# Performance work log

Hardware: AMD Instinct MI355X
Metric: run time of the kernel (lower is better)

Reference implementation:

```python
import jax, jax.numpy as jnp
import numpy as np

B, T, S, H, N = 4, 1024, 1024, 1024, 16
D = H // N
EPS = 1e-12
MASK_FILL = -1e6


def setup_inputs() -> dict:
    key = jax.random.key(0)
    ks = jax.random.split(key, 20)
    w = lambda i: jax.random.normal(ks[i], (H, H), jnp.float32) * 0.02
    zb = jnp.zeros((H,), jnp.float32)
    tgt_mask = jnp.tile(jnp.tril(jnp.ones((T, T), jnp.int32))[None], (B, 1, 1))
    return {
        "encoder_states": jax.random.normal(ks[0], (B, S, H), jnp.float32),
        "decoder_inputs": jax.random.normal(ks[1], (B, T, H), jnp.float32),
        "src_attn_mask": jnp.ones((B, S), jnp.int32),
        "tgt_attn_mask": tgt_mask,
        "q_w": w(2), "q_b": zb,
        "k_w": w(3), "k_b": zb,
        "v_w": w(4), "v_b": zb,
        "sq_w": w(5), "sq_b": zb,
        "sk_w": w(6), "sk_b": zb,
        "sv_w": w(7), "sv_b": zb,
        "dense_w": w(8), "dense_b": zb,
        "ln_g": jnp.ones((H,), jnp.float32),
        "ln_b": zb,
    }


def _layernorm(x, g, b):
    mu = jnp.mean(x, -1, keepdims=True)
    var = jnp.mean(jnp.square(x - mu), -1, keepdims=True)
    return (x - mu) * jax.lax.rsqrt(var + EPS) * g + b


def _attention(q, k, v, mask, dense_w, dense_b, ln_g, ln_b):
    # q:[B,Q,H] k,v:[B,K,H]; NOTE: original applies NO 1/sqrt(d) scaling.
    b, qlen, _ = q.shape
    klen = k.shape[1]
    qh = q.reshape(b, qlen, N, D).transpose(0, 2, 1, 3)  # [B,N,Q,D]
    kh = k.reshape(b, klen, N, D).transpose(0, 2, 1, 3)
    vh = v.reshape(b, klen, N, D).transpose(0, 2, 1, 3)
    scores = jnp.einsum('bnqd,bnkd->bnqk', qh, kh)
    m = mask.reshape(b, 1, qlen, klen) if mask.ndim == 3 else mask.reshape(b, 1, 1, klen)
    scores = jnp.where(m == 0, jnp.asarray(MASK_FILL, scores.dtype), scores)
    probs = jax.nn.softmax(scores, axis=-1)  # dropout = identity at eval
    ctx = jnp.einsum('bnqk,bnkd->bqnd', probs, vh)  # [B,Q,N,D]
    w = dense_w.T.reshape(N, D, H)
    proj = jnp.einsum('bqnd,ndh->bqh', ctx, w) + dense_b
    # Residual is q (the query projection), faithful to the original code.
    return _layernorm(q + proj, ln_g, ln_b)


def reference(encoder_states, decoder_inputs, src_attn_mask, tgt_attn_mask,
              q_w, q_b, k_w, k_b, v_w, v_b,
              sq_w, sq_b, sk_w, sk_b, sv_w, sv_b,
              dense_w, dense_b, ln_g, ln_b):
    lin = lambda x, w, b: x @ w.T + b
    # self-attention over decoder inputs
    q = lin(decoder_inputs, q_w, q_b)
    k = lin(decoder_inputs, k_w, k_b)
    v = lin(decoder_inputs, v_w, v_b)
    self_out = _attention(q, k, v, tgt_attn_mask, dense_w, dense_b, ln_g, ln_b)
    # cross-attention into encoder states (same dense/LayerNorm modules)
    q2 = lin(self_out, sq_w, sq_b)
    k2 = lin(encoder_states, sk_w, sk_b)
    v2 = lin(encoder_states, sv_w, sv_b)
    return _attention(q2, k2, v2, src_attn_mask, dense_w, dense_b, ln_g, ln_b)
```

## Files before the change

kernel.cpp:

```cpp
#include <hip/hip_runtime.h>

typedef __attribute__((ext_vector_type(4))) float f32x4;
typedef __attribute__((ext_vector_type(8))) short bf16x8;

#define GVOID const __attribute__((address_space(1))) void
#define LVOID __attribute__((address_space(3))) void

__device__ __forceinline__ float bf2f(ushort u){
  union { float f; unsigned int i; } c; c.i = ((unsigned int)u) << 16; return c.f;
}
__device__ __forceinline__ ushort f2bf(float f){
  union { float f; unsigned int i; } c; c.f = f;
  unsigned int r = (c.i + 0x7FFFu + ((c.i >> 16) & 1u)) >> 16;
  return (ushort)r;
}

struct CvtArgs {
  const float* s[9];
  ushort*      d[9];
  int          blks[9];
};
__global__ __launch_bounds__(256) void cvtk_multi(CvtArgs ca){
  int bid = blockIdx.x;
  int seg = 0, base = 0;
  while (bid - base >= ca.blks[seg]){ base += ca.blks[seg]; ++seg; }
  int i = ((bid - base) * 256 + threadIdx.x) * 4;
  float4 v = *(const float4*)(ca.s[seg] + i);
  ushort4 o;
  o.x = f2bf(v.x); o.y = f2bf(v.y); o.z = f2bf(v.z); o.w = f2bf(v.w);
  *(ushort4*)(ca.d[seg] + i) = o;
}

struct GemmArgs {
  const ushort* A[3];
  const ushort* W[3];
  const float*  bias[3];
  const ushort* R[3];
  ushort*       C[3];
  int           mode[3];
};

__global__ __launch_bounds__(256,2) void gemm128(GemmArgs ga, int nmat, int N, int K){
  __shared__ ushort As[128 * 64];
  __shared__ ushort Bs[128 * 64];
  const int ntn = N >> 7;
  const int per = ntn * nmat;
  const int x = blockIdx.x & 7, ii = blockIdx.x >> 3;
  const int ipx = gridDim.x >> 3;
  const int gpx = ipx / per;
  const int tm = x * gpx + ii / per;
  const int q = ii % per;
  const int g = q / ntn, tn = q % ntn;
  const ushort* __restrict__ A = ga.A[g];
  const ushort* __restrict__ W = ga.W[g];
  const float*  __restrict__ bias = ga.bias[g];
  const ushort* __restrict__ R = ga.R[g];
  ushort* __restrict__ C = ga.C[g];
  const int mode = ga.mode[g];

  const int t = threadIdx.x, lane = t & 63, wave = t >> 6;
  const int wr = wave >> 1, wc = wave & 1;
  const int l15 = lane & 15, l4 = lane >> 4;
  const int rowBase = tm * 128, colBase = tn * 128;

  f32x4 acc[4][4] = {};
  const int NT = K >> 6;
  for (int tk = 0; tk < NT; ++tk){
    const int k0 = tk * 64;
    __syncthreads();
#pragma unroll
    for (int j = 0; j < 4; ++j){
      int cb = j * 256 + wave * 64 + lane;
      int row = cb >> 3;
      int kc = (cb & 7) ^ (row & 7);
      const ushort* srcA = A + (size_t)(rowBase + row) * K + k0 + kc * 8;
      __builtin_amdgcn_global_load_lds((GVOID*)srcA, (LVOID*)(As + (size_t)cb * 8), 16, 0, 0);
      const ushort* srcB = W + (size_t)(colBase + row) * K + k0 + kc * 8;
      __builtin_amdgcn_global_load_lds((GVOID*)srcB, (LVOID*)(Bs + (size_t)cb * 8), 16, 0, 0);
    }
    __syncthreads();
#pragma unroll
    for (int kk = 0; kk < 2; ++kk){
      bf16x8 a[4], b[4];
#pragma unroll
      for (int m = 0; m < 4; ++m){
        int row = wr * 64 + m * 16 + l15;
        int ch = row * 8 + ((kk * 4 + l4) ^ (row & 7));
        a[m] = *(const bf16x8*)(As + ch * 8);
      }
#pragma unroll
      for (int n = 0; n < 4; ++n){
        int row = wc * 64 + n * 16 + l15;
        int ch = row * 8 + ((kk * 4 + l4) ^ (row & 7));
        b[n] = *(const bf16x8*)(Bs + ch * 8);
      }
#pragma unroll
      for (int m = 0; m < 4; ++m)
#pragma unroll
      for (int n = 0; n < 4; ++n)
        acc[m][n] = __builtin_amdgcn_mfma_f32_16x16x32_bf16(a[m], b[n], acc[m][n], 0, 0, 0);
    }
  }
#pragma unroll
  for (int m = 0; m < 4; ++m)
#pragma unroll
  for (int n = 0; n < 4; ++n)
#pragma unroll
  for (int r = 0; r < 4; ++r){
    int row = rowBase + wr * 64 + m * 16 + l4 * 4 + r;
    int col = colBase + wc * 64 + n * 16 + l15;
    float v = acc[m][n][r] + bias[col];
    if (mode == 1) v += bf2f(R[(size_t)row * N + col]);
    if (mode == 2){
      int bb = row >> 10, tt = row & 1023, nh = col >> 6, d = col & 63;
      C[((size_t)((bb * 16 + nh) * 64 + d)) * 1024 + tt] = f2bf(v);
    } else {
      C[(size_t)row * N + col] = f2bf(v);
    }
  }
}

__global__ __launch_bounds__(256,2) void gemm_bt(GemmArgs ga, int nmat, int M, int N, int K){
  __shared__ ushort As[2][128 * 64];
  __shared__ ushort Bs[2][64 * 64];
  const int nb = gridDim.x;
  const int ntn = N >> 6;
  const int tq_cnt = ntn * nmat;
  const int x = blockIdx.x & 7, ii = blockIdx.x >> 3;
  const int ipx = nb >> 3;
  const int gpx = ipx / tq_cnt;
  const int tm = x * gpx + ii / tq_cnt;
  const int tq = ii % tq_cnt;
  const int g = tq / ntn, tn = tq % ntn;
  const ushort* __restrict__ A = ga.A[g];
  const ushort* __restrict__ W = ga.W[g];
  const float*  __restrict__ bias = ga.bias[g];
  const ushort* __restrict__ R = ga.R[g];
  ushort* __restrict__ C = ga.C[g];
  const int mode = ga.mode[g];

  const int t = threadIdx.x, lane = t & 63, wave = t >> 6;
  const int wr = wave >> 1, wc = wave & 1;
  const int l15 = lane & 15, l4 = lane >> 4;
  const int rowBase = tm * 128, colBase = tn * 64;

  auto stage = [&](int buf, int k0){
#pragma unroll
    for (int j = 0; j < 4; ++j){
      int cb = j * 256 + wave * 64;
      int p = cb + lane;
      int row = p >> 3;
      int kc = (p & 7) ^ (row & 7);
      const ushort* src = A + (size_t)(rowBase + row) * K + k0 + kc * 8;
      __builtin_amdgcn_global_load_lds((GVOID*)src, (LVOID*)(&As[buf][cb * 8]), 16, 0, 0);
    }
#pragma unroll
    for (int j = 0; j < 2; ++j){
      int cb = j * 256 + wave * 64;
      int p = cb + lane;
      int row = p >> 3;
      int kc = (p & 7) ^ (row & 7);
      const ushort* src = W + (size_t)(colBase + row) * K + k0 + kc * 8;
      __builtin_amdgcn_global_load_lds((GVOID*)src, (LVOID*)(&Bs[buf][cb * 8]), 16, 0, 0);
    }
  };

  f32x4 acc[4][2] = {};
  const int NT = K >> 6;
  stage(0, 0);
  __syncthreads();
  for (int tk = 0; tk < NT; ++tk){
    const int cur = tk & 1;
    if (tk + 1 < NT) stage(cur ^ 1, (tk + 1) * 64);
#pragma unroll
    for (int kk = 0; kk < 2; ++kk){
      bf16x8 a[4], b[2];
#pragma unroll
      for (int m = 0; m < 4; ++m){
        int row = wr * 64 + m * 16 + l15;
        int ch = row * 8 + kk * 4 + l4;
        ch ^= (row & 7);
        a[m] = *(const bf16x8*)(&As[cur][ch * 8]);
      }
#pragma unroll
      for (int n = 0; n < 2; ++n){
        int row = wc * 32 + n * 16 + l15;
        int ch = row * 8 + kk * 4 + l4;
        ch ^= (row & 7);
        b[n] = *(const bf16x8*)(&Bs[cur][ch * 8]);
      }
#pragma unroll
      for (int m = 0; m < 4; ++m)
#pragma unroll
      for (int n = 0; n < 2; ++n)
        acc[m][n] = __builtin_amdgcn_mfma_f32_16x16x32_bf16(a[m], b[n], acc[m][n], 0, 0, 0);
    }
    __syncthreads();
  }
#pragma unroll
  for (int m = 0; m < 4; ++m)
#pragma unroll
  for (int n = 0; n < 2; ++n)
#pragma unroll
  for (int r = 0; r < 4; ++r){
    int row = rowBase + wr * 64 + m * 16 + l4 * 4 + r;
    int col = colBase + wc * 32 + n * 16 + l15;
    float v = acc[m][n][r] + bias[col];
    if (mode == 1) v += bf2f(R[(size_t)row * N + col]);
    if (mode == 2){
      int bb = row >> 10, tt = row & 1023, nh = col >> 6, d = col & 63;
      C[((size_t)((bb * 16 + nh) * 64 + d)) * 1024 + tt] = f2bf(v);
    } else {
      C[(size_t)row * N + col] = f2bf(v);
    }
  }
}

__global__ __launch_bounds__(256,2) void attn_kernel(const ushort* __restrict__ Q, const ushort* __restrict__ Kv,
    const ushort* __restrict__ Vt, ushort* __restrict__ O, const int* __restrict__ smask, int causal){
  __shared__ ushort Ks[2][64 * 64];
  __shared__ ushort Vs[2][64 * 64];
  __shared__ __align__(16) char Ps[4][4096];
  const int p = blockIdx.x;
  const int x = p & 7, j = p >> 3;
  const int gg = x * 8 + (j & 7);
  const int b = gg >> 4, head = gg & 15;
  const int c3 = (j >> 3) & 3, rr = j >> 5;
  const int qt = causal ? (rr ? (7 - c3) : c3) : (j >> 3);
  const int t = threadIdx.x, lane = t & 63, wave = t >> 6;
  const int l15 = lane & 15, l4 = lane >> 4;
  const int qr0 = qt * 128 + wave * 32;
  const int sw = (l15 & 7) << 3;

  bf16x8 aq[2][2];
#pragma unroll
  for (int m = 0; m < 2; ++m)
#pragma unroll
  for (int kk = 0; kk < 2; ++kk)
    aq[m][kk] = *(const bf16x8*)(Q + (size_t)(b * 1024 + qr0 + m * 16 + l15) * 1024 + head * 64 + kk * 32 + l4 * 8);

  f32x4 cacc[2][4] = {};
  float mrow[2] = {-1e30f, -1e30f}, lrow[2] = {0.f, 0.f};

  auto stage = [&](int buf, int k0){
#pragma unroll
    for (int jj = 0; jj < 2; ++jj){
      int cb = jj * 256 + wave * 64;
      int pp = cb + lane;
      int row = pp >> 3;
      int kc = (pp & 7) ^ (row & 7);
      const ushort* src = Kv + (size_t)(b * 1024 + k0 + row) * 1024 + head * 64 + kc * 8;
      __builtin_amdgcn_global_load_lds((GVOID*)src, (LVOID*)(&Ks[buf][cb * 8]), 16, 0, 0);
    }
#pragma unroll
    for (int jj = 0; jj < 2; ++jj){
      int cb = jj * 256 + wave * 64;
      int pp = cb + lane;
      int row = pp >> 3;
      int kc = (pp & 7) ^ (row & 7);
      const ushort* src = Vt + (size_t)((b * 16 + head) * 64 + row) * 1024 + k0 + kc * 8;
      __builtin_amdgcn_global_load_lds((GVOID*)src, (LVOID*)(&Vs[buf][cb * 8]), 16, 0, 0);
    }
  };

  const int nkt = causal ? (2 * qt + 2) : 16;
  stage(0, 0);
  __syncthreads();
  char* Pb = &Ps[wave][0];
  for (int kt = 0; kt < nkt; ++kt){
    const int cur = kt & 1;
    const int k0 = kt * 64;
    if (kt + 1 < nkt) stage(cur ^ 1, (kt + 1) * 64);
    const ushort* Kb_ = &Ks[cur][0];
    const ushort* Vb_ = &Vs[cur][0];
    f32x4 st[2][4] = {};
#pragma unroll
    for (int kk = 0; kk < 2; ++kk){
      bf16x8 ak[4];
#pragma unroll
      for (int n = 0; n < 4; ++n){
        int row = n * 16 + l15;
        int ch = row * 8 + ((kk * 4 + l4) ^ (row & 7));
        ak[n] = *(const bf16x8*)(Kb_ + ch * 8);
      }
#pragma unroll
      for (int m = 0; m < 2; ++m)
#pragma unroll
      for (int n = 0; n < 4; ++n)
        st[m][n] = __builtin_amdgcn_mfma_f32_16x16x32_bf16(ak[n], aq[m][kk], st[m][n], 0, 0, 0);
    }
    if (causal && k0 + 63 > qr0){
#pragma unroll
      for (int m = 0; m < 2; ++m)
#pragma unroll
      for (int n = 0; n < 4; ++n)
#pragma unroll
      for (int r = 0; r < 4; ++r)
        if (k0 + n * 16 + l4 * 4 + r > qr0 + m * 16 + l15) st[m][n][r] = -1e6f;
    }
    if (smask){
#pragma unroll
      for (int n = 0; n < 4; ++n)
#pragma unroll
      for (int r = 0; r < 4; ++r){
        int mv = smask[b * 1024 + k0 + n * 16 + l4 * 4 + r];
        if (mv == 0){ st[0][n][r] = -1e6f; st[1][n][r] = -1e6f; }
      }
    }
    float scal[2];
#pragma unroll
    for (int m = 0; m < 2; ++m){
      float mx = st[m][0][0];
#pragma unroll
      for (int n = 0; n < 4; ++n)
#pragma unroll
      for (int r = 0; r < 4; ++r) mx = fmaxf(mx, st[m][n][r]);
      mx = fmaxf(mx, __shfl_xor(mx, 16));
      mx = fmaxf(mx, __shfl_xor(mx, 32));
      float mn = fmaxf(mrow[m], mx);
      scal[m] = __expf(mrow[m] - mn);
      mrow[m] = mn;
      float ps = 0.f;
#pragma unroll
      for (int n = 0; n < 4; ++n)
#pragma unroll
      for (int r = 0; r < 4; ++r){
        float pv = __expf(st[m][n][r] - mn);
        st[m][n][r] = pv;
        ps += pv;
      }
      ps += __shfl_xor(ps, 16);
      ps += __shfl_xor(ps, 32);
      lrow[m] = lrow[m] * scal[m] + ps;
    }
#pragma unroll
    for (int m = 0; m < 2; ++m)
#pragma unroll
    for (int r = 0; r < 4; ++r){
      float sb = __shfl(scal[m], l4 * 4 + r);
#pragma unroll
      for (int nd = 0; nd < 4; ++nd) cacc[m][nd][r] *= sb;
    }
#pragma unroll
    for (int m = 0; m < 2; ++m)
#pragma unroll
    for (int n = 0; n < 4; ++n){
      unsigned lo = (unsigned)f2bf(st[m][n][0]) | ((unsigned)f2bf(st[m][n][1]) << 16);
      unsigned hi = (unsigned)f2bf(st[m][n][2]) | ((unsigned)f2bf(st[m][n][3]) << 16);
      unsigned long long pk = (unsigned long long)lo | ((unsigned long long)hi << 32);
      *(unsigned long long*)(Pb + m * 2048 + l15 * 128 + ((n * 32 + l4 * 8) ^ sw)) = pk;
    }
#pragma unroll
    for (int ks = 0; ks < 2; ++ks){
      bf16x8 bv[4];
#pragma unroll
      for (int nd = 0; nd < 4; ++nd){
        int row = nd * 16 + l15;
        int ch = row * 8 + ((ks * 4 + l4) ^ (row & 7));
        bv[nd] = *(const bf16x8*)(Vb_ + ch * 8);
      }
#pragma unroll
      for (int m = 0; m < 2; ++m){
        int base = m * 2048 + l15 * 128;
        int o = ks * 64 + l4 * 16;
        union { bf16x8 v; unsigned long long u[2]; } pa;
        pa.u[0] = *(const unsigned long long*)(Pb + base + ((o    ) ^ sw));
        pa.u[1] = *(const unsigned long long*)(Pb + base + ((o + 8) ^ sw));
#pragma unroll
        for (int nd = 0; nd < 4; ++nd)
          cacc[m][nd] = __builtin_amdgcn_mfma_f32_16x16x32_bf16(pa.v, bv[nd], cacc[m][nd], 0, 0, 0);
      }
    }
    __syncthreads();
  }
#pragma unroll
  for (int m = 0; m < 2; ++m)
#pragma unroll
  for (int r = 0; r < 4; ++r){
    float lb = __shfl(lrow[m], l4 * 4 + r);
    float inv = 1.f / lb;
    int row = qr0 + m * 16 + l4 * 4 + r;
#pragma unroll
    for (int nd = 0; nd < 4; ++nd){
      int col = head * 64 + nd * 16 + l15;
      O[(size_t)(b * 1024 + row) * 1024 + col] = f2bf(cacc[m][nd][r] * inv);
    }
  }
}

__global__ __launch_bounds__(256) void ln_kernel(const ushort* __restrict__ X, const float* __restrict__ g,
    const float* __restrict__ bta, ushort* __restrict__ outb, float* __restrict__ outf){
  const int row = blockIdx.x, t = threadIdx.x;
  const ushort* xr = X + (size_t)row * 1024;
  ushort4 u = *(const ushort4*)(xr + t * 4);
  float x0 = bf2f(u.x), x1 = bf2f(u.y), x2 = bf2f(u.z), x3 = bf2f(u.w);
  float s = x0 + x1 + x2 + x3;
  float s2 = x0 * x0 + x1 * x1 + x2 * x2 + x3 * x3;
#pragma unroll
  for (int d = 1; d < 64; d <<= 1){ s += __shfl_xor(s, d); s2 += __shfl_xor(s2, d); }
  __shared__ float red[8];
  const int lane = t & 63, wave = t >> 6;
  if (lane == 0){ red[wave] = s; red[4 + wave] = s2; }
  __syncthreads();
  s = red[0] + red[1] + red[2] + red[3];
  s2 = red[4] + red[5] + red[6] + red[7];
  float mu = s * (1.f / 1024.f);
  float var = fmaxf(s2 * (1.f / 1024.f) - mu * mu, 0.f);
  float rstd = rsqrtf(var + 1e-12f);
  int col = t * 4;
  float y0 = (x0 - mu) * rstd * g[col + 0] + bta[col + 0];
  float y1 = (x1 - mu) * rstd * g[col + 1] + bta[col + 1];
  float y2 = (x2 - mu) * rstd * g[col + 2] + bta[col + 2];
  float y3 = (x3 - mu) * rstd * g[col + 3] + bta[col + 3];
  if (outb){
    ushort4 o; o.x = f2bf(y0); o.y = f2bf(y1); o.z = f2bf(y2); o.w = f2bf(y3);
    *(ushort4*)(outb + (size_t)row * 1024 + col) = o;
  } else {
    float4 o; o.x = y0; o.y = y1; o.z = y2; o.w = y3;
    *(float4*)(outf + (size_t)row * 1024 + col) = o;
  }
}

extern "C" void kernel_launch(void* const* d_in, const int* in_sizes, int n_in,
                              void* d_out, int out_size, void* d_ws, size_t ws_size,
                              hipStream_t stream){
  const float* enc = (const float*)d_in[0];
  const float* dec = (const float*)d_in[1];
  const int* smask = (const int*)d_in[2];
  const float* q_w  = (const float*)d_in[4];  const float* q_b  = (const float*)d_in[5];
  const float* k_w  = (const float*)d_in[6];  const float* k_b  = (const float*)d_in[7];
  const float* v_w  = (const float*)d_in[8];  const float* v_b  = (const float*)d_in[9];
  const float* sq_w = (const float*)d_in[10]; const float* sq_b = (const float*)d_in[11];
  const float* sk_w = (const float*)d_in[12]; const float* sk_b = (const float*)d_in[13];
  const float* sv_w = (const float*)d_in[14]; const float* sv_b = (const float*)d_in[15];
  const float* dw   = (const float*)d_in[16]; const float* db   = (const float*)d_in[17];
  const float* lng  = (const float*)d_in[18]; const float* lnb  = (const float*)d_in[19];
  ushort* ws = (ushort*)d_ws;
  const size_t MEG = 1024u * 1024u;
  ushort* decb = ws + 0 * MEG;
  ushort* encb = ws + 4 * MEG;
  ushort* Qb   = ws + 8 * MEG;
  ushort* Kb   = ws + 12 * MEG;
  ushort* Vtb  = ws + 20 * MEG;
  ushort* ctx  = ws + 24 * MEG;
  ushort* S1   = ws + 28 * MEG;
  ushort* Wq  = ws + 32 * MEG; ushort* Wk  = ws + 33 * MEG; ushort* Wv  = ws + 34 * MEG;
  ushort* Wsq = ws + 35 * MEG; ushort* Wsk = ws + 36 * MEG; ushort* Wsv = ws + 37 * MEG;
  ushort* Wd  = ws + 38 * MEG;
  const int M = 4096, N = 1024, Kd = 1024;
  {
    CvtArgs ca;
    ca.s[0] = dec;  ca.d[0] = decb; ca.blks[0] = 4096;
    ca.s[1] = enc;  ca.d[1] = encb; ca.blks[1] = 4096;
    ca.s[2] = q_w;  ca.d[2] = Wq;   ca.blks[2] = 1024;
    ca.s[3] = k_w;  ca.d[3] = Wk;   ca.blks[3] = 1024;
    ca.s[4] = v_w;  ca.d[4] = Wv;   ca.blks[4] = 1024;
    ca.s[5] = sq_w; ca.d[5] = Wsq;  ca.blks[5] = 1024;
    ca.s[6] = sk_w; ca.d[6] = Wsk;  ca.blks[6] = 1024;
    ca.s[7] = sv_w; ca.d[7] = Wsv;  ca.blks[7] = 1024;
    ca.s[8] = dw;   ca.d[8] = Wd;   ca.blks[8] = 1024;
    cvtk_multi<<<15360, 256, 0, stream>>>(ca);
  }
  {
    GemmArgs ga;
    ga.A[0] = decb; ga.A[1] = decb; ga.A[2] = decb;
    ga.W[0] = Wq;   ga.W[1] = Wk;   ga.W[2] = Wv;
    ga.bias[0] = q_b; ga.bias[1] = k_b; ga.bias[2] = v_b;
    ga.R[0] = nullptr; ga.R[1] = nullptr; ga.R[2] = nullptr;
    ga.C[0] = Qb;   ga.C[1] = Kb;   ga.C[2] = Vtb;
    ga.mode[0] = 0; ga.mode[1] = 0; ga.mode[2] = 2;
    gemm128<<<768, 256, 0, stream>>>(ga, 3, N, Kd);
  }
  attn_kernel<<<512, 256, 0, stream>>>(Qb, Kb, Vtb, ctx, nullptr, 1);
  {
    GemmArgs ga = {};
    ga.A[0] = ctx; ga.W[0] = Wd; ga.bias[0] = db; ga.R[0] = Qb; ga.C[0] = S1; ga.mode[0] = 1;
    gemm_bt<<<512, 256, 0, stream>>>(ga, 1, M, N, Kd);
  }
  ln_kernel<<<4096, 256, 0, stream>>>(S1, lng, lnb, decb, nullptr);
  {
    GemmArgs ga;
    ga.A[0] = decb; ga.A[1] = encb; ga.A[2] = encb;
    ga.W[0] = Wsq;  ga.W[1] = Wsk;  ga.W[2] = Wsv;
    ga.bias[0] = sq_b; ga.bias[1] = sk_b; ga.bias[2] = sv_b;
    ga.R[0] = nullptr; ga.R[1] = nullptr; ga.R[2] = nullptr;
    ga.C[0] = Qb;   ga.C[1] = Kb;   ga.C[2] = Vtb;
    ga.mode[0] = 0; ga.mode[1] = 0; ga.mode[2] = 2;
    gemm128<<<768, 256, 0, stream>>>(ga, 3, N, Kd);
  }
  attn_kernel<<<512, 256, 0, stream>>>(Qb, Kb, Vtb, ctx, smask, 0);
  {
    GemmArgs ga = {};
    ga.A[0] = ctx; ga.W[0] = Wd; ga.bias[0] = db; ga.R[0] = Qb; ga.C[0] = S1; ga.mode[0] = 1;
    gemm_bt<<<512, 256, 0, stream>>>(ga, 1, M, N, Kd);
  }
  ln_kernel<<<4096, 256, 0, stream>>>(S1, lng, lnb, nullptr, (float*)d_out);
}
```

Before: 225.0 us.

## Halve attention query tile, fold log2e into Q projection, use exp2 softmax

Attention blocks now cover 64 query rows instead of 128, with one 16-row slice per wave. The grid doubles to 1024 blocks and launch bounds allow 4 blocks per CU, with a new causal tile ordering for load balance. The Q projection is pre-scaled by log2(e) so softmax can use the hardware exp2 directly; the residual in the dense GEMM is rescaled by ln2 to undo this, and the mask fill becomes -1.5e6 to match. Probabilities are packed with v_cvt_pk_bf16_f32, and the unused residual/transposed-store paths are dropped from the GEMM epilogues. The risk is that each K/V tile is loaded for fewer query rows, and the bf16-rounded scaled Q differs slightly numerically.

```diff
diff --git a/kernel.cpp b/kernel.cpp
--- a/kernel.cpp
+++ b/kernel.cpp
@@ -5,6 +5,9 @@
 
 #define GVOID const __attribute__((address_space(1))) void
 #define LVOID __attribute__((address_space(3))) void
+
+#define LOG2E 1.44269504f
+#define LN2   0.69314718f
 
 __device__ __forceinline__ float bf2f(ushort u){
   union { float f; unsigned int i; } c; c.i = ((unsigned int)u) << 16; return c.f;
@@ -38,6 +41,7 @@
   const ushort* R[3];
   ushort*       C[3];
   int           mode[3];
+  float         scale[3];
 };
 
 __global__ __launch_bounds__(256,2) void gemm128(GemmArgs ga, int nmat, int N, int K){
@@ -54,9 +58,9 @@
   const ushort* __restrict__ A = ga.A[g];
   const ushort* __restrict__ W = ga.W[g];
   const float*  __restrict__ bias = ga.bias[g];
-  const ushort* __restrict__ R = ga.R[g];
   ushort* __restrict__ C = ga.C[g];
   const int mode = ga.mode[g];
+  const float scale = ga.scale[g];
 
   const int t = threadIdx.x, lane = t & 63, wave = t >> 6;
   const int wr = wave >> 1, wc = wave & 1;
@@ -109,8 +113,7 @@
   for (int r = 0; r < 4; ++r){
     int row = rowBase + wr * 64 + m * 16 + l4 * 4 + r;
     int col = colBase + wc * 64 + n * 16 + l15;
-    float v = acc[m][n][r] + bias[col];
-    if (mode == 1) v += bf2f(R[(size_t)row * N + col]);
+    float v = (acc[m][n][r] + bias[col]) * scale;
     if (mode == 2){
       int bb = row >> 10, tt = row & 1023, nh = col >> 6, d = col & 63;
       C[((size_t)((bb * 16 + nh) * 64 + d)) * 1024 + tt] = f2bf(v);
@@ -206,41 +209,38 @@
     int row = rowBase + wr * 64 + m * 16 + l4 * 4 + r;
     int col = colBase + wc * 32 + n * 16 + l15;
     float v = acc[m][n][r] + bias[col];
-    if (mode == 1) v += bf2f(R[(size_t)row * N + col]);
-    if (mode == 2){
-      int bb = row >> 10, tt = row & 1023, nh = col >> 6, d = col & 63;
-      C[((size_t)((bb * 16 + nh) * 64 + d)) * 1024 + tt] = f2bf(v);
-    } else {
-      C[(size_t)row * N + col] = f2bf(v);
-    }
-  }
-}
-
-__global__ __launch_bounds__(256,2) void attn_kernel(const ushort* __restrict__ Q, const ushort* __restrict__ Kv,
+    if (mode == 1) v += bf2f(R[(size_t)row * N + col]) * LN2;
+    C[(size_t)row * N + col] = f2bf(v);
+  }
+}
+
+__global__ __launch_bounds__(256,4) void attn_kernel(const ushort* __restrict__ Q, const ushort* __restrict__ Kv,
     const ushort* __restrict__ Vt, ushort* __restrict__ O, const int* __restrict__ smask, int causal){
   __shared__ ushort Ks[2][64 * 64];
   __shared__ ushort Vs[2][64 * 64];
-  __shared__ __align__(16) char Ps[4][4096];
+  __shared__ __align__(16) char Ps[4][2048];
   const int p = blockIdx.x;
   const int x = p & 7, j = p >> 3;
   const int gg = x * 8 + (j & 7);
   const int b = gg >> 4, head = gg & 15;
-  const int c3 = (j >> 3) & 3, rr = j >> 5;
-  const int qt = causal ? (rr ? (7 - c3) : c3) : (j >> 3);
+  const int rr = j >> 3;
+  int qt;
+  if (causal){
+    int lo = rr & 3, hi = rr >> 2;
+    qt = (hi == 0) ? lo * 2 : (hi == 1) ? lo * 2 + 1 : (hi == 2) ? 15 - lo * 2 : 14 - lo * 2;
+  } else qt = rr;
   const int t = threadIdx.x, lane = t & 63, wave = t >> 6;
   const int l15 = lane & 15, l4 = lane >> 4;
-  const int qr0 = qt * 128 + wave * 32;
+  const int qr0 = qt * 64 + wave * 16;
   const int sw = (l15 & 7) << 3;
 
-  bf16x8 aq[2][2];
-#pragma unroll
-  for (int m = 0; m < 2; ++m)
+  bf16x8 aq[2];
 #pragma unroll
   for (int kk = 0; kk < 2; ++kk)
-    aq[m][kk] = *(const bf16x8*)(Q + (size_t)(b * 1024 + qr0 + m * 16 + l15) * 1024 + head * 64 + kk * 32 + l4 * 8);
-
-  f32x4 cacc[2][4] = {};
-  float mrow[2] = {-1e30f, -1e30f}, lrow[2] = {0.f, 0.f};
+    aq[kk] = *(const bf16x8*)(Q + (size_t)(b * 1024 + qr0 + l15) * 1024 + head * 64 + kk * 32 + l4 * 8);
+
+  f32x4 cacc[4] = {};
+  float mrow = -1e30f, lrow = 0.f;
 
   auto stage = [&](int buf, int k0){
 #pragma unroll
@@ -263,7 +263,7 @@
     }
   };
 
-  const int nkt = causal ? (2 * qt + 2) : 16;
+  const int nkt = causal ? (qt + 1) : 16;
   stage(0, 0);
   __syncthreads();
   char* Pb = &Ps[wave][0];
@@ -273,7 +273,7 @@
     if (kt + 1 < nkt) stage(cur ^ 1, (kt + 1) * 64);
     const ushort* Kb_ = &Ks[cur][0];
     const ushort* Vb_ = &Vs[cur][0];
-    f32x4 st[2][4] = {};
+    f32x4 st[4] = {};
 #pragma unroll
     for (int kk = 0; kk < 2; ++kk){
       bf16x8 ak[4];
@@ -284,19 +284,15 @@
         ak[n] = *(const bf16x8*)(Kb_ + ch * 8);
       }
 #pragma unroll
-      for (int m = 0; m < 2; ++m)
-#pragma unroll
       for (int n = 0; n < 4; ++n)
-        st[m][n] = __builtin_amdgcn_mfma_f32_16x16x32_bf16(ak[n], aq[m][kk], st[m][n], 0, 0, 0);
+        st[n] = __builtin_amdgcn_mfma_f32_16x16x32_bf16(ak[n], aq[kk], st[n], 0, 0, 0);
     }
     if (causal && k0 + 63 > qr0){
 #pragma unroll
-      for (int m = 0; m < 2; ++m)
-#pragma unroll
       for (int n = 0; n < 4; ++n)
 #pragma unroll
       for (int r = 0; r < 4; ++r)
-        if (k0 + n * 16 + l4 * 4 + r > qr0 + m * 16 + l15) st[m][n][r] = -1e6f;
+        if (k0 + n * 16 + l4 * 4 + r > qr0 + l15) st[n][r] = -1.5e6f;
     }
     if (smask){
 #pragma unroll
@@ -304,51 +300,44 @@
 #pragma unroll
       for (int r = 0; r < 4; ++r){
         int mv = smask[b * 1024 + k0 + n * 16 + l4 * 4 + r];
-        if (mv == 0){ st[0][n][r] = -1e6f; st[1][n][r] = -1e6f; }
-      }
-    }
-    float scal[2];
-#pragma unroll
-    for (int m = 0; m < 2; ++m){
-      float mx = st[m][0][0];
-#pragma unroll
-      for (int n = 0; n < 4; ++n)
-#pragma unroll
-      for (int r = 0; r < 4; ++r) mx = fmaxf(mx, st[m][n][r]);
-      mx = fmaxf(mx, __shfl_xor(mx, 16));
-      mx = fmaxf(mx, __shfl_xor(mx, 32));
-      float mn = fmaxf(mrow[m], mx);
-      scal[m] = __expf(mrow[m] - mn);
-      mrow[m] = mn;
-      float ps = 0.f;
-#pragma unroll
-      for (int n = 0; n < 4; ++n)
-#pragma unroll
-      for (int r = 0; r < 4; ++r){
-        float pv = __expf(st[m][n][r] - mn);
-        st[m][n][r] = pv;
-        ps += pv;
-      }
-      ps += __shfl_xor(ps, 16);
-      ps += __shfl_xor(ps, 32);
-      lrow[m] = lrow[m] * scal[m] + ps;
-    }
-#pragma unroll
-    for (int m = 0; m < 2; ++m)
+        if (mv == 0) st[n][r] = -1.5e6f;
+      }
+    }
+    float mx = st[0][0];
+#pragma unroll
+    for (int n = 0; n < 4; ++n)
+#pragma unroll
+    for (int r = 0; r < 4; ++r) mx = fmaxf(mx, st[n][r]);
+    mx = fmaxf(mx, __shfl_xor(mx, 16));
+    mx = fmaxf(mx, __shfl_xor(mx, 32));
+    float mn = fmaxf(mrow, mx);
+    float scal = __builtin_amdgcn_exp2f(mrow - mn);
+    mrow = mn;
+    float ps = 0.f;
+#pragma unroll
+    for (int n = 0; n < 4; ++n)
 #pragma unroll
     for (int r = 0; r < 4; ++r){
-      float sb = __shfl(scal[m], l4 * 4 + r);
-#pragma unroll
-      for (int nd = 0; nd < 4; ++nd) cacc[m][nd][r] *= sb;
-    }
-#pragma unroll
-    for (int m = 0; m < 2; ++m)
+      float pv = __builtin_amdgcn_exp2f(st[n][r] - mn);
+      st[n][r] = pv;
+      ps += pv;
+    }
+    ps += __shfl_xor(ps, 16);
+    ps += __shfl_xor(ps, 32);
+    lrow = lrow * scal + ps;
+#pragma unroll
+    for (int r = 0; r < 4; ++r){
+      float sb = __shfl(scal, l4 * 4 + r);
+#pragma unroll
+      for (int nd = 0; nd < 4; ++nd) cacc[nd][r] *= sb;
+    }
 #pragma unroll
     for (int n = 0; n < 4; ++n){
-      unsigned lo = (unsigned)f2bf(st[m][n][0]) | ((unsigned)f2bf(st[m][n][1]) << 16);
-      unsigned hi = (unsigned)f2bf(st[m][n][2]) | ((unsigned)f2bf(st[m][n][3]) << 16);
-      unsigned long long pk = (unsigned long long)lo | ((unsigned long long)hi << 32);
-      *(unsigned long long*)(Pb + m * 2048 + l15 * 128 + ((n * 32 + l4 * 8) ^ sw)) = pk;
+      unsigned lo_, hi_;
+      asm("v_cvt_pk_bf16_f32 %0, %1, %2" : "=v"(lo_) : "v"(st[n][0]), "v"(st[n][1]));
+      asm("v_cvt_pk_bf16_f32 %0, %1, %2" : "=v"(hi_) : "v"(st[n][2]), "v"(st[n][3]));
+      unsigned long long pk = (unsigned long long)lo_ | ((unsigned long long)hi_ << 32);
+      *(unsigned long long*)(Pb + l15 * 128 + ((n * 32 + l4 * 8) ^ sw)) = pk;
     }
 #pragma unroll
     for (int ks = 0; ks < 2; ++ks){
@@ -359,31 +348,26 @@
         int ch = row * 8 + ((ks * 4 + l4) ^ (row & 7));
         bv[nd] = *(const bf16x8*)(Vb_ + ch * 8);
       }
-#pragma unroll
-      for (int m = 0; m < 2; ++m){
-        int base = m * 2048 + l15 * 128;
-        int o = ks * 64 + l4 * 16;
-        union { bf16x8 v; unsigned long long u[2]; } pa;
-        pa.u[0] = *(const unsigned long long*)(Pb + base + ((o    ) ^ sw));
-        pa.u[1] = *(const unsigned long long*)(Pb + base + ((o + 8) ^ sw));
-#pragma unroll
-        for (int nd = 0; nd < 4; ++nd)
-          cacc[m][nd] = __builtin_amdgcn_mfma_f32_16x16x32_bf16(pa.v, bv[nd], cacc[m][nd], 0, 0, 0);
-      }
+      int base = l15 * 128;
+      int o = ks * 64 + l4 * 16;
+      union { bf16x8 v; unsigned long long u[2]; } pa;
+      pa.u[0] = *(const unsigned long long*)(Pb + base + ((o    ) ^ sw));
+      pa.u[1] = *(const unsigned long long*)(Pb + base + ((o + 8) ^ sw));
+#pragma unroll
+      for (int nd = 0; nd < 4; ++nd)
+        cacc[nd] = __builtin_amdgcn_mfma_f32_16x16x32_bf16(pa.v, bv[nd], cacc[nd], 0, 0, 0);
     }
     __syncthreads();
   }
 #pragma unroll
-  for (int m = 0; m < 2; ++m)
-#pragma unroll
   for (int r = 0; r < 4; ++r){
-    float lb = __shfl(lrow[m], l4 * 4 + r);
+    float lb = __shfl(lrow, l4 * 4 + r);
     float inv = 1.f / lb;
-    int row = qr0 + m * 16 + l4 * 4 + r;
+    int row = qr0 + l4 * 4 + r;
 #pragma unroll
     for (int nd = 0; nd < 4; ++nd){
       int col = head * 64 + nd * 16 + l15;
-      O[(size_t)(b * 1024 + row) * 1024 + col] = f2bf(cacc[m][nd][r] * inv);
+      O[(size_t)(b * 1024 + row) * 1024 + col] = f2bf(cacc[nd][r] * inv);
     }
   }
 }
@@ -469,12 +453,14 @@
     ga.R[0] = nullptr; ga.R[1] = nullptr; ga.R[2] = nullptr;
     ga.C[0] = Qb;   ga.C[1] = Kb;   ga.C[2] = Vtb;
     ga.mode[0] = 0; ga.mode[1] = 0; ga.mode[2] = 2;
+    ga.scale[0] = LOG2E; ga.scale[1] = 1.f; ga.scale[2] = 1.f;
     gemm128<<<768, 256, 0, stream>>>(ga, 3, N, Kd);
   }
-  attn_kernel<<<512, 256, 0, stream>>>(Qb, Kb, Vtb, ctx, nullptr, 1);
+  attn_kernel<<<1024, 256, 0, stream>>>(Qb, Kb, Vtb, ctx, nullptr, 1);
   {
     GemmArgs ga = {};
     ga.A[0] = ctx; ga.W[0] = Wd; ga.bias[0] = db; ga.R[0] = Qb; ga.C[0] = S1; ga.mode[0] = 1;
+    ga.scale[0] = 1.f;
     gemm_bt<<<512, 256, 0, stream>>>(ga, 1, M, N, Kd);
   }
   ln_kernel<<<4096, 256, 0, stream>>>(S1, lng, lnb, decb, nullptr);
@@ -486,12 +472,14 @@
     ga.R[0] = nullptr; ga.R[1] = nullptr; ga.R[2] = nullptr;
     ga.C[0] = Qb;   ga.C[1] = Kb;   ga.C[2] = Vtb;
     ga.mode[0] = 0; ga.mode[1] = 0; ga.mode[2] = 2;
+    ga.scale[0] = LOG2E; ga.scale[1] = 1.f; ga.scale[2] = 1.f;
     gemm128<<<768, 256, 0, stream>>>(ga, 3, N, Kd);
   }
-  attn_kernel<<<512, 256, 0, stream>>>(Qb, Kb, Vtb, ctx, smask, 0);
+  attn_kernel<<<1024, 256, 0, stream>>>(Qb, Kb, Vtb, ctx, smask, 0);
   {
     GemmArgs ga = {};
     ga.A[0] = ctx; ga.W[0] = Wd; ga.bias[0] = db; ga.R[0] = Qb; ga.C[0] = S1; ga.mode[0] = 1;
+    ga.scale[0] = 1.f;
     gemm_bt<<<512, 256, 0, stream>>>(ga, 1, M, N, Kd);
   }
   ln_kernel<<<4096, 256, 0, stream>>>(S1, lng, lnb, nullptr, (float*)d_out);
```

After: 213.0 us. -5.3%, faster.
